# Kernel tuning notes

Measured on AMD Instinct MI355X. Metric: run time of the kernel, lower is better.

Reference implementation:

```python
import jax, jax.numpy as jnp
import numpy as np
from jax import lax

V = 9; C1 = 80; C2 = 40; C4 = 24; CH = 32
H1, W1 = 30, 40; H2, W2 = 60, 80; H4, W4 = 120, 160
SHAPE = (96, 96, 96); N = 131072; EPS = 1e-5
OFFS = np.stack(np.meshgrid(np.arange(-1, 2), np.arange(-1, 2), np.arange(-1, 2), indexing='ij'), -1).reshape(-1, 3).astype(np.int32)  # 27 kernel offsets


def conv2d(x, w, b):
    y = lax.conv_general_dilated(x, w, (1, 1), 'SAME', dimension_numbers=('NCHW', 'OIHW', 'NCHW'))
    return y + b[None, :, None, None]


def bn1d(x, g, b):  # eval-mode BatchNorm1d (running_mean=0, running_var=1)
    return g * x * (1.0 / np.sqrt(1.0 + EPS)) + b


def layernorm(x, g, b):
    m = x.mean(-1, keepdims=True)
    v = ((x - m) ** 2).mean(-1, keepdims=True)
    return (x - m) / jnp.sqrt(v + EPS) * g + b


def grid_sample_zeros(img, gx, gy):
    # img [V,C,H,W]; gx,gy [V,M] normalized to [-1,1]; bilinear, align_corners=True, zeros padding
    Vn, C, H, W = img.shape
    px = (gx + 1.0) * 0.5 * (W - 1)
    py = (gy + 1.0) * 0.5 * (H - 1)
    x0 = jnp.floor(px); y0 = jnp.floor(py)
    wx = px - x0; wy = py - y0
    flat = img.reshape(Vn, C, H * W)
    def corner(xc, yc, wgt):
        valid = (xc >= 0) & (xc <= W - 1) & (yc >= 0) & (yc <= H - 1)
        xi = jnp.clip(xc, 0, W - 1).astype(jnp.int32)
        yi = jnp.clip(yc, 0, H - 1).astype(jnp.int32)
        idx = yi * W + xi  # [V,M]
        g = jax.vmap(lambda f, i: f[:, i])(flat, idx)  # [V,C,M]
        return g * (wgt * valid)[:, None, :]
    return (corner(x0, y0, (1 - wx) * (1 - wy)) + corner(x0 + 1, y0, wx * (1 - wy))
            + corner(x0, y0 + 1, (1 - wx) * wy) + corner(x0 + 1, y0 + 1, wx * wy))


def subm_conv(feat, W3, cxyz, grid):
    # submanifold sparse 3x3x3 conv: per-offset gather of active neighbors -> GEMM -> accumulate
    n = feat.shape[0]
    shp = jnp.asarray(SHAPE, jnp.int32)
    out = jnp.zeros((n, W3.shape[-1]), feat.dtype)
    for k in range(27):
        nc = cxyz + jnp.asarray(OFFS[k])
        inb = jnp.all((nc >= 0) & (nc < shp), axis=1)
        ncc = jnp.clip(nc, 0, shp - 1)
        idx = grid[ncc[:, 0], ncc[:, 1], ncc[:, 2]]
        ok = (inb & (idx >= 0)).astype(feat.dtype)
        g = feat[jnp.clip(idx, 0, n - 1)] * ok[:, None]
        out = out + g @ W3[k]
    return out


def _forward(feats_1x, feats_2x, feats_4x, origin, voxel_size, KRcam,
             w_f1, b_f1, w_f2, b_f2, w_f4, b_f4, w_down, b_down,
             w_p1, b_p1, w_p2, b_p2, w_p3, b_p3, w_p4, b_p4,
             bn0_g, bn0_b, w_elan, w_s1, ln1_g, ln1_b, w_s2, ln2_g, ln2_b,
             w_s3, ln3_g, ln3_b, w_s4, bn4_g, bn4_b,
             coords, stage, min_view_number):
    # feat_fusion_pre (bs=1, take batch 0)
    f1 = jax.nn.relu(conv2d(feats_1x[:, 0], w_f1, b_f1))
    f2 = jax.nn.relu(conv2d(feats_2x[:, 0], w_f2, b_f2))
    f4 = jax.nn.relu(conv2d(feats_4x[:, 0], w_f4, b_f4))
    f1 = jax.image.resize(f1, (V, C1, H2, W2), 'bilinear')  # F.interpolate x2
    f4 = f4.reshape(V, C4, H2, 2, W2, 2).mean(axis=(3, 5))  # AvgPool2d(2)
    fuse = jnp.concatenate([f1, f2, f4], axis=1)
    fuse = jax.nn.relu(conv2d(fuse, w_down, b_down))
    for w, b in ((w_p1, b_p1), (w_p2, b_p2), (w_p3, b_p3), (w_p4, b_p4)):
        fuse = fuse + jax.nn.relu(conv2d(fuse, w, b))  # residual blocks -> [V,CH,H2,W2]
    # multi-view projection
    cxyz = coords[:, 1:]
    world = cxyz.astype(jnp.float32) * voxel_size + origin[0]
    hom = jnp.concatenate([world, jnp.ones_like(world[:, :1])], axis=1)  # [N,4]
    im_p = jnp.einsum('vij,nj->vin', KRcam[:, 0], hom)  # [V,3,N]
    im_z = im_p[:, 2]
    gx = 2.0 * (im_p[:, 0] / im_z) / (W4 - 1) - 1.0
    gy = 2.0 * (im_p[:, 1] / im_z) / (H4 - 1) - 1.0
    mask = (jnp.abs(gx) <= 1) & (jnp.abs(gy) <= 1) & (im_z > 0)  # [V,N]
    count = mask.sum(0).astype(jnp.float32)
    # inputs are constructed so every voxel is seen by all views: valid_voxel compaction == identity
    feats = grid_sample_zeros(fuse, gx, gy) * mask[:, None, :]  # [V,CH,N]
    feat = feats.transpose(2, 0, 1)  # [N,V,CH]
    m = mask.T.astype(feat.dtype)  # [N,V]
    den = m.sum(1, keepdims=True)
    mean = (m[..., None] * feat).sum(1) / den
    var = (m[..., None] * (feat - mean[:, None, :]) ** 2).sum(1) / den  # [N,CH]
    # sparse subm conv chain
    sc = cxyz // (2 ** (2 - stage))  # stage=2 -> identity
    grid = jnp.full(SHAPE, -1, jnp.int32).at[sc[:, 0], sc[:, 1], sc[:, 2]].set(jnp.arange(N, dtype=jnp.int32))
    x = bn1d(var, bn0_g, bn0_b)
    x = jax.nn.relu(subm_conv(x, w_elan, sc, grid))  # Spares3dELAN stand-in
    r = jax.nn.relu(subm_conv(x, w_s1, sc, grid)); x = layernorm(r + x, ln1_g, ln1_b)
    r = jax.nn.relu(subm_conv(x, w_s2, sc, grid)); x = layernorm(r + x, ln2_g, ln2_b)
    r = jax.nn.relu(subm_conv(x, w_s3, sc, grid)); x = layernorm(r + x, ln3_g, ln3_b)
    occ = bn1d(subm_conv(x, w_s4, sc, grid), bn4_g, bn4_b)  # [N,1]
    return occ, coords, count


def setup_inputs() -> dict:
    key = jax.random.key(0)
    keys = jax.random.split(key, 40)
    ki = iter(range(40))
    def rn(shape, s=1.0):
        return jax.random.normal(keys[next(ki)], shape, jnp.float32) * s
    inp = {}
    inp['feats_1x'] = rn((V, 1, C1, H1, W1))
    inp['feats_2x'] = rn((V, 1, C2, H2, W2))
    inp['feats_4x'] = rn((V, 1, C4, H4, W4))
    flat = np.arange(N, dtype=np.int64) * 6  # unique active voxels in a 96^3 grid
    cx = flat // (96 * 96); rem = flat % (96 * 96)
    inp['coords'] = jnp.asarray(np.stack([np.zeros(N, np.int64), cx, rem // 96, rem % 96], 1), jnp.int32)
    inp['origin'] = jnp.asarray([[-1.92, -1.92, 1.0]], jnp.float32)
    inp['voxel_size'] = jnp.float32(0.04)
    fx, fy = 38.0, 28.0
    P = np.zeros((V, 1, 3, 4), np.float32)
    for v in range(V):
        P[v, 0] = np.array([[fx, 0.0, (W4 - 1) / 2, fx * 0.02 * (v - 4)],
                            [0.0, fy, (H4 - 1) / 2, 0.0],
                            [0.0, 0.0, 1.0, 0.0]], np.float32)
    inp['KRcam'] = jnp.asarray(P)
    s = 0.05
    inp['w_f1'] = rn((C1, C1, 3, 3), s); inp['b_f1'] = rn((C1,), s)
    inp['w_f2'] = rn((C2, C2, 3, 3), s); inp['b_f2'] = rn((C2,), s)
    inp['w_f4'] = rn((C4, C4, 3, 3), s); inp['b_f4'] = rn((C4,), s)
    inp['w_down'] = rn((CH, C1 + C2 + C4, 1, 1), s); inp['b_down'] = rn((CH,), s)
    for i in (1, 2, 3, 4):
        inp['w_p%d' % i] = rn((CH, CH, 3, 3), s); inp['b_p%d' % i] = rn((CH,), s)
    inp['bn0_g'] = jnp.ones((CH,), jnp.float32); inp['bn0_b'] = jnp.zeros((CH,), jnp.float32)
    inp['w_elan'] = rn((27, CH, CH), s)
    inp['w_s1'] = rn((27, CH, CH), s); inp['ln1_g'] = jnp.ones((CH,), jnp.float32); inp['ln1_b'] = jnp.zeros((CH,), jnp.float32)
    inp['w_s2'] = rn((27, CH, CH), s); inp['ln2_g'] = jnp.ones((CH,), jnp.float32); inp['ln2_b'] = jnp.zeros((CH,), jnp.float32)
    inp['w_s3'] = rn((27, CH, CH), s); inp['ln3_g'] = jnp.ones((CH,), jnp.float32); inp['ln3_b'] = jnp.zeros((CH,), jnp.float32)
    inp['w_s4'] = rn((27, CH, 1), s); inp['bn4_g'] = jnp.ones((1,), jnp.float32); inp['bn4_b'] = jnp.zeros((1,), jnp.float32)
    inp['stage'] = 2
    inp['min_view_number'] = 1
    return inp


def reference(feats_1x, feats_2x, feats_4x, origin, voxel_size, KRcam,
              w_f1, b_f1, w_f2, b_f2, w_f4, b_f4, w_down, b_down,
              w_p1, b_p1, w_p2, b_p2, w_p3, b_p3, w_p4, b_p4,
              bn0_g, bn0_b, w_elan, w_s1, ln1_g, ln1_b, w_s2, ln2_g, ln2_b,
              w_s3, ln3_g, ln3_b, w_s4, bn4_g, bn4_b,
              coords, stage, min_view_number):
    return _forward(feats_1x, feats_2x, feats_4x, origin, voxel_size, KRcam,
                    w_f1, b_f1, w_f2, b_f2, w_f4, b_f4, w_down, b_down,
                    w_p1, b_p1, w_p2, b_p2, w_p3, b_p3, w_p4, b_p4,
                    bn0_g, bn0_b, w_elan, w_s1, ln1_g, ln1_b, w_s2, ln2_g, ln2_b,
                    w_s3, ln3_g, ln3_b, w_s4, bn4_g, bn4_b,
                    coords, stage, min_view_number)
```

## Files before the change

### kernel.cpp

```cpp
#include <hip/hip_runtime.h>
#include <math.h>

#define VN 9
#define NVOX 131072
#define GS 96
static constexpr float INVS = 0.9999950000374997f;

typedef short bf16x8 __attribute__((ext_vector_type(8)));
typedef float f32x4v __attribute__((ext_vector_type(4)));

__device__ inline float4 ld4(const float* p){ return *reinterpret_cast<const float4*>(p); }

__device__ inline ushort f2b(float f){
  unsigned u = __float_as_uint(f);
  unsigned r = (u + 0x7fffu + ((u >> 16) & 1u)) >> 16;
  return (ushort)r;
}
__device__ inline float b2f(ushort s){ return __uint_as_float(((unsigned)s) << 16); }
__device__ inline float blo(unsigned u){ return __uint_as_float(u << 16); }
__device__ inline float bhi(unsigned u){ return __uint_as_float(u & 0xffff0000u); }

__device__ inline float4 ld4b(const ushort* p){
  uint2 u = *reinterpret_cast<const uint2*>(p);
  float4 r; r.x = blo(u.x); r.y = bhi(u.x); r.z = blo(u.y); r.w = bhi(u.y); return r;
}
__device__ inline void st4b(ushort* p, float4 v){
  uint2 u;
  u.x = (unsigned)f2b(v.x) | ((unsigned)f2b(v.y) << 16);
  u.y = (unsigned)f2b(v.z) | ((unsigned)f2b(v.w) << 16);
  *reinterpret_cast<uint2*>(p) = u;
}

__device__ inline void wprep2_dev(const float* __restrict__ w, ushort* __restrict__ o,
                                  int Cout, int Cin, int K, int CK, int CoutPad, int tid){
  int ci32 = tid & 31;
  int co = (tid >> 5) % CoutPad;
  int ck = (tid / (32*CoutPad)) % CK;
  int tap = tid / (32*CoutPad*CK);
  int ci = ck*32 + ci32;
  float v = 0.f;
  if (co < Cout && ci < Cin) v = w[(size_t)(co*Cin + ci)*K*K + tap];
  o[tid] = f2b(v);
}
__device__ inline void wprep_dev(const float* __restrict__ w, ushort* __restrict__ o, int tid){
  int k = tid >> 10;
  int r = tid & 1023;
  int co = r >> 5;
  int ci = r & 31;
  o[tid] = f2b(w[k*1024 + ci*32 + co]);
}

__device__ inline void nhwc_tile_dev(const float* __restrict__ in, ushort* __restrict__ out,
                                     int C, int Cpad, int HW, int tile, int tilesPerV,
                                     float* lds, int tx){
  int v  = tile / tilesPerV;
  int p0 = (tile - v*tilesPerV) * 64;
  const float* ip = in + (size_t)v*C*HW + p0;
  int iters = Cpad >> 2;
  for (int i = 0; i < iters; ++i){
    int idx = i*256 + tx;
    int c = idx >> 6;
    int p = idx & 63;
    float val = 0.f;
    if (c < C && (p0 + p) < HW) val = ip[(size_t)c*HW + p];
    lds[c*65 + p] = val;
  }
  __syncthreads();
  int groups = Cpad >> 2;
  int tot = 64*groups;
  for (int basei = 0; basei < tot; basei += 256){
    int idx = basei + tx;
    if (idx < tot){
      int g  = idx % groups;
      int px = idx / groups;
      if ((p0 + px) < HW){
        float4 r;
        r.x = lds[(g*4+0)*65 + px];
        r.y = lds[(g*4+1)*65 + px];
        r.z = lds[(g*4+2)*65 + px];
        r.w = lds[(g*4+3)*65 + px];
        st4b(out + (size_t)(v*HW + p0 + px)*Cpad + g*4, r);
      }
    }
  }
}

__global__ __launch_bounds__(256) void k_prep(
    const float* wf1s, const float* wf2s, const float* wf4s, const float* wdns,
    const float* wp0s, const float* wp1s, const float* wp2s, const float* wp3s,
    const float* wes, const float* ws1s, const float* ws2s, const float* ws3s,
    ushort* wf1, ushort* wf2, ushort* wf4, ushort* wdn,
    ushort* wp0, ushort* wp1, ushort* wp2, ushort* wp3,
    ushort* w2e, ushort* w2s1, ushort* w2s2, ushort* w2s3,
    int* grid,
    const float* f1, const float* f2, const float* f4,
    ushort* o1, ushort* o2, ushort* o4){
  __shared__ float lds[96*65];
  int bid = blockIdx.x;
  int tx = threadIdx.x;
  if (bid < 270){ int t = bid*256+tx; if (t < 69120) wprep2_dev(wf1s, wf1, 80, 80, 3, 3, 80, t); return; }
  bid -= 270;
  if (bid < 108){ int t = bid*256+tx; if (t < 27648) wprep2_dev(wf2s, wf2, 40, 40, 3, 2, 48, t); return; }
  bid -= 108;
  if (bid < 36){ int t = bid*256+tx; if (t < 9216) wprep2_dev(wf4s, wf4, 24, 24, 3, 1, 32, t); return; }
  bid -= 36;
  if (bid < 20){ int t = bid*256+tx; if (t < 5120) wprep2_dev(wdns, wdn, 32, 144, 1, 5, 32, t); return; }
  bid -= 20;
  if (bid < 36){ int t = bid*256+tx; if (t < 9216) wprep2_dev(wp0s, wp0, 32, 32, 3, 1, 32, t); return; }
  bid -= 36;
  if (bid < 36){ int t = bid*256+tx; if (t < 9216) wprep2_dev(wp1s, wp1, 32, 32, 3, 1, 32, t); return; }
  bid -= 36;
  if (bid < 36){ int t = bid*256+tx; if (t < 9216) wprep2_dev(wp2s, wp2, 32, 32, 3, 1, 32, t); return; }
  bid -= 36;
  if (bid < 36){ int t = bid*256+tx; if (t < 9216) wprep2_dev(wp3s, wp3, 32, 32, 3, 1, 32, t); return; }
  bid -= 36;
  if (bid < 108){ int t = bid*256+tx; if (t < 27648) wprep_dev(wes, w2e, t); return; }
  bid -= 108;
  if (bid < 108){ int t = bid*256+tx; if (t < 27648) wprep_dev(ws1s, w2s1, t); return; }
  bid -= 108;
  if (bid < 108){ int t = bid*256+tx; if (t < 27648) wprep_dev(ws2s, w2s2, t); return; }
  bid -= 108;
  if (bid < 108){ int t = bid*256+tx; if (t < 27648) wprep_dev(ws3s, w2s3, t); return; }
  bid -= 108;
  if (bid < 3456){ int t = bid*256+tx; if (t < GS*GS*GS) grid[t] = -1; return; }
  bid -= 3456;
  if (bid < 171){ nhwc_tile_dev(f1, o1, 80, 96, 1200, bid, 19, lds, tx); return; }
  bid -= 171;
  if (bid < 675){ nhwc_tile_dev(f2, o2, 40, 64, 4800, bid, 75, lds, tx); return; }
  bid -= 675;
  if (bid < 2700){ nhwc_tile_dev(f4, o4, 24, 32, 19200, bid, 300, lds, tx); }
}

template<int CK, int NT, int TAPS, int MT>
__device__ void conv_dev(
    const ushort* __restrict__ fin, const ushort* __restrict__ w2,
    const float* __restrict__ bias, ushort* __restrict__ outp,
    int H, int W, int total, int Cout, int outStride, int outOff,
    const ushort* __restrict__ skipin, int bid, int tid){
  constexpr int CIN = CK*32;
  constexpr int COP = NT*16;
  int lane = tid & 63;
  int wave = tid >> 6;
  int vbase = bid*(MT*64) + wave*(MT*16);
  int m = lane & 15, q = lane >> 4;
  int HW = H*W;
  int p[MT], py[MT], px[MT]; bool pin[MT];
  #pragma unroll
  for (int t = 0; t < MT; ++t){
    int pp = vbase + t*16 + m;
    pin[t] = pp < total;
    if (pp > total-1) pp = total-1;
    p[t] = pp;
    int v = pp / HW; int rem = pp - v*HW;
    int y = rem / W;
    py[t] = y; px[t] = rem - y*W;
  }
  f32x4v acc[MT][NT];
  #pragma unroll
  for (int t = 0; t < MT; ++t)
    #pragma unroll
    for (int n = 0; n < NT; ++n) acc[t][n] = 0.f;
  bf16x8 z = (short)0;

  #pragma unroll 1
  for (int tap = 0; tap < TAPS; ++tap){
    int dy = (TAPS == 9) ? tap/3 - 1 : 0;
    int dx = (TAPS == 9) ? tap%3 - 1 : 0;
    int off = dy*W + dx;
    bool val[MT];
    #pragma unroll
    for (int t = 0; t < MT; ++t)
      val[t] = pin[t] && ((unsigned)(py[t]+dy) < (unsigned)H)
                      && ((unsigned)(px[t]+dx) < (unsigned)W);
    #pragma unroll
    for (int ck = 0; ck < CK; ++ck){
      bf16x8 Af[MT], Bf[NT];
      #pragma unroll
      for (int t = 0; t < MT; ++t){
        size_t idx = val[t] ? (size_t)(p[t]+off) : 0;
        bf16x8 a = *(const bf16x8*)(fin + idx*CIN + ck*32 + q*8);
        Af[t] = val[t] ? a : z;
      }
      #pragma unroll
      for (int n = 0; n < NT; ++n)
        Bf[n] = *(const bf16x8*)(w2 + ((size_t)((tap*CK+ck)*COP + n*16 + m))*32 + q*8);
      #pragma unroll
      for (int t = 0; t < MT; ++t)
        #pragma unroll
        for (int n = 0; n < NT; ++n)
          acc[t][n] = __builtin_amdgcn_mfma_f32_16x16x32_bf16(Af[t], Bf[n], acc[t][n], 0, 0, 0);
    }
  }

  #pragma unroll
  for (int n = 0; n < NT; ++n){
    int co = n*16 + m;
    bool cok = co < Cout;
    float bs = cok ? bias[co] : 0.f;
    #pragma unroll
    for (int t = 0; t < MT; ++t){
      #pragma unroll
      for (int r = 0; r < 4; ++r){
        int pp = vbase + t*16 + q*4 + r;
        if (pp < total && cok){
          float x = fmaxf(acc[t][n][r] + bs, 0.f);
          if (skipin) x += b2f(skipin[(size_t)pp*CIN + co]);
          outp[(size_t)pp*outStride + outOff + co] = f2b(x);
        }
      }
    }
  }
}

template<int CK, int NT, int TAPS, int MT>
__global__ __launch_bounds__(256) void k_conv_mfma(
    const ushort* __restrict__ fin, const ushort* __restrict__ w2,
    const float* __restrict__ bias, ushort* __restrict__ outp,
    int H, int W, int total, int Cout, int outStride, int outOff,
    const ushort* __restrict__ skipin){
  conv_dev<CK,NT,TAPS,MT>(fin, w2, bias, outp, H, W, total, Cout, outStride, outOff,
                          skipin, blockIdx.x, threadIdx.x);
}

template<int TH, int NT>
__device__ void conv_lds_dev(
    const ushort* __restrict__ fin, const ushort* __restrict__ w2,
    const float* __restrict__ bias, ushort* __restrict__ outp,
    int H, int W, int Cout, int outStride,
    const ushort* __restrict__ skipin, ushort* lds, int bid, int tid){
  constexpr int RPW = TH/4;
  constexpr int PS = 36;
  int xtiles = W >> 4;
  int ytiles = (H + TH - 1) / TH;
  int v  = bid / (ytiles*xtiles);
  int rem = bid - v*(ytiles*xtiles);
  int ty = (rem / xtiles) * TH;
  int tx = (rem % xtiles) * 16;
  const ushort* ibase = fin + (size_t)v*H*W*32;
  for (int i = tid; i < (TH+2)*18*4; i += 256){
    int chunk = i & 3;
    int pxi = i >> 2;
    int ly = pxi / 18, lx = pxi - ly*18;
    int gy = ty + ly - 1, gx = tx + lx - 1;
    uint4 d = {0,0,0,0};
    if ((unsigned)gy < (unsigned)H && (unsigned)gx < (unsigned)W)
      d = *(const uint4*)(ibase + ((size_t)gy*W + gx)*32 + chunk*8);
    *(uint4*)(lds + (size_t)(ly*18 + lx)*PS + chunk*8) = d;
  }
  __syncthreads();
  int lane = tid & 63;
  int wave = tid >> 6;
  int m = lane & 15, q = lane >> 4;
  f32x4v acc[RPW][NT];
  #pragma unroll
  for (int t = 0; t < RPW; ++t)
    #pragma unroll
    for (int n = 0; n < NT; ++n) acc[t][n] = 0.f;

  #pragma unroll 1
  for (int tap = 0; tap < 9; ++tap){
    int dy = tap/3 - 1, dx = tap%3 - 1;
    bf16x8 Af[RPW], Bf[NT];
    #pragma unroll
    for (int t = 0; t < RPW; ++t){
      int ly = wave*RPW + t + 1 + dy;
      int lx = m + 1 + dx;
      Af[t] = *(const bf16x8*)(lds + (size_t)(ly*18 + lx)*PS + q*8);
    }
    #pragma unroll
    for (int n = 0; n < NT; ++n)
      Bf[n] = *(const bf16x8*)(w2 + ((size_t)(tap*(NT*16) + n*16 + m))*32 + q*8);
    #pragma unroll
    for (int t = 0; t < RPW; ++t)
      #pragma unroll
      for (int n = 0; n < NT; ++n)
        acc[t][n] = __builtin_amdgcn_mfma_f32_16x16x32_bf16(Af[t], Bf[n], acc[t][n], 0, 0, 0);
  }

  #pragma unroll
  for (int n = 0; n < NT; ++n){
    int co = n*16 + m;
    bool cok = co < Cout;
    float bs = cok ? bias[co] : 0.f;
    #pragma unroll
    for (int t = 0; t < RPW; ++t){
      int y = ty + wave*RPW + t;
      #pragma unroll
      for (int r = 0; r < 4; ++r){
        int x = tx + q*4 + r;
        if (y < H && cok){
          size_t pp = (size_t)(v*H + y)*W + x;
          float val = fmaxf(acc[t][n][r] + bs, 0.f);
          if (skipin) val += b2f(skipin[pp*32 + co]);
          outp[pp*outStride + co] = f2b(val);
        }
      }
    }
  }
}

__global__ __launch_bounds__(256) void k_conv_lds4(
    const ushort* __restrict__ fin, const ushort* __restrict__ w2,
    const float* __restrict__ bias, ushort* __restrict__ outp,
    const ushort* __restrict__ skipin){
  __shared__ ushort lds[6*18*36];
  conv_lds_dev<4,2>(fin, w2, bias, outp, 60, 80, 32, 32, skipin, lds, blockIdx.x, threadIdx.x);
}

__device__ void scatter_dev(const int* __restrict__ coords, const int* __restrict__ stage,
                            int* __restrict__ grid, int* __restrict__ scn,
                            float* __restrict__ coords_out,
                            const float* __restrict__ origin, const float* __restrict__ vsz,
                            const float* __restrict__ KR,
                            ushort* __restrict__ sidx, uint2* __restrict__ sw,
                            float* __restrict__ cnt, int n){
  int c0 = coords[n*4], c1 = coords[n*4+1], c2 = coords[n*4+2], c3 = coords[n*4+3];
  coords_out[n*4+0] = (float)c0;
  coords_out[n*4+1] = (float)c1;
  coords_out[n*4+2] = (float)c2;
  coords_out[n*4+3] = (float)c3;
  int sh = 2 - stage[0];
  int s1 = c1 >> sh, s2 = c2 >> sh, s3 = c3 >> sh;
  scn[n*3+0] = s1; scn[n*3+1] = s2; scn[n*3+2] = s3;
  grid[(s1*GS + s2)*GS + s3] = n;

  float vs = vsz[0];
  float wx = (float)c1*vs + origin[0];
  float wy = (float)c2*vs + origin[1];
  float wz = (float)c3*vs + origin[2];
  float den = 0.f;
  #pragma unroll 1
  for (int v = 0; v < VN; ++v){
    const float* P = KR + v*12;
    float ix = P[0]*wx + P[1]*wy + P[2]*wz + P[3];
    float iy = P[4]*wx + P[5]*wy + P[6]*wz + P[7];
    float iz = P[8]*wx + P[9]*wy + P[10]*wz + P[11];
    float gx = 2.f*(ix/iz)/159.f - 1.f;
    float gy = 2.f*(iy/iz)/119.f - 1.f;
    bool ok = (fabsf(gx) <= 1.f) && (fabsf(gy) <= 1.f) && (iz > 0.f);
    float px = ok ? (gx + 1.f)*0.5f*79.f : 0.f;
    float py = ok ? (gy + 1.f)*0.5f*59.f : 0.f;
    float x0f = floorf(px), y0f = floorf(py);
    float fx = px - x0f, fy = py - y0f;
    int idx = (int)y0f*80 + (int)x0f;
    float mf = ok ? 1.f : 0.f;
    float w00 = (1.f-fx)*(1.f-fy)*mf, w01 = fx*(1.f-fy)*mf;
    float w10 = (1.f-fx)*fy*mf,       w11 = fx*fy*mf;
    uint2 s;
    s.x = (unsigned)f2b(w00) | ((unsigned)f2b(w01) << 16);
    s.y = (unsigned)f2b(w10) | ((unsigned)f2b(w11) << 16);
    sidx[(size_t)v*NVOX + n] = (ushort)idx;
    sw[(size_t)v*NVOX + n] = s;
    den += mf;
  }
  cnt[n] = den;
}

__global__ __launch_bounds__(256) void k_heads(
    const ushort* nhwc1, const ushort* wf1, const float* b_f1, ushort* t1,
    const ushort* nhwc2, const ushort* wf2, const float* b_f2, ushort* fcat,
    const ushort* nhwc4, const ushort* wf4, const float* b_f4, ushort* t4,
    const int* coords, const int* stage, int* grid, int* scn, float* coords_out,
    const float* origin, const float* vsz, const float* KR,
    ushort* sidx, uint2* sw, float* cnt){
  __shared__ ushort lds[18*18*36];
  int bid = blockIdx.x;
  int tid = threadIdx.x;
  if (bid < 169){ conv_dev<3,5,9,1>(nhwc1, wf1, b_f1, t1, 30, 40, 10800, 80, 80, 0, nullptr, bid, tid); return; }
  bid -= 169;
  if (bid < 720){ conv_lds_dev<16,2>(nhwc4, wf4, b_f4, t4, 120, 160, 24, 24, nullptr, lds, bid, tid); return; }
  bid -= 720;
  if (bid < 675){ conv_dev<2,3,9,1>(nhwc2, wf2, b_f2, fcat, 60, 80, 43200, 40, 160, 80, nullptr, bid, tid); return; }
  bid -= 675;
  { int n = bid*256 + tid;
    scatter_dev(coords, stage, grid, scn, coords_out, origin, vsz, KR, sidx, sw, cnt, n); }
}

__global__ __launch_bounds__(256) void k_respool_nbr(
    const ushort* __restrict__ t1, const ushort* __restrict__ t4, ushort* __restrict__ fc,
    const int* __restrict__ scn, const int* __restrict__ grid,
    int* __restrict__ nbr, unsigned* __restrict__ gmask16){
  __shared__ unsigned m16[4];
  int bid = blockIdx.x;
  int tidx = threadIdx.x;
  if (bid < 5063){
    int tid = bid*256 + tidx;
    if (tid < 864000){
      int c4 = tid % 20;
      int x  = (tid / 20) % 80;
      int y  = (tid / 1600) % 60;
      int v  = tid / 96000;
      int c = c4*4;
      int ky = y >> 1; int y0, y1; float wy0, wy1;
      if ((y & 1) == 0){ y0 = ky-1; y1 = ky; wy0 = 0.25f; wy1 = 0.75f; if (y0 < 0){ y0 = 0; wy0 = 0.f; wy1 = 1.f; } }
      else             { y0 = ky; y1 = ky+1; wy0 = 0.75f; wy1 = 0.25f; if (y1 > 29){ y1 = 29; wy1 = 0.f; wy0 = 1.f; } }
      int kx = x >> 1; int x0, x1; float wx0, wx1;
      if ((x & 1) == 0){ x0 = kx-1; x1 = kx; wx0 = 0.25f; wx1 = 0.75f; if (x0 < 0){ x0 = 0; wx0 = 0.f; wx1 = 1.f; } }
      else             { x0 = kx; x1 = kx+1; wx0 = 0.75f; wx1 = 0.25f; if (x1 > 39){ x1 = 39; wx1 = 0.f; wx0 = 1.f; } }
      float4 a00 = ld4b(t1 + ((size_t)(v*30 + y0)*40 + x0)*80 + c);
      float4 a01 = ld4b(t1 + ((size_t)(v*30 + y0)*40 + x1)*80 + c);
      float4 a10 = ld4b(t1 + ((size_t)(v*30 + y1)*40 + x0)*80 + c);
      float4 a11 = ld4b(t1 + ((size_t)(v*30 + y1)*40 + x1)*80 + c);
      float w00 = wy0*wx0, w01 = wy0*wx1, w10 = wy1*wx0, w11 = wy1*wx1;
      float4 r;
      r.x = w00*a00.x + w01*a01.x + w10*a10.x + w11*a11.x;
      r.y = w00*a00.y + w01*a01.y + w10*a10.y + w11*a11.y;
      r.z = w00*a00.z + w01*a01.z + w10*a10.z + w11*a11.z;
      r.w = w00*a00.w + w01*a01.w + w10*a10.w + w11*a11.w;
      st4b(fc + ((size_t)(v*60 + y)*80 + x)*160 + c, r);
      return;
    }
    int t = tid - 864000;
    if (t >= 432000) return;
    int c4 = t % 10;
    int x  = (t / 10) % 80;
    int y  = (t / 800) % 60;
    int v  = t / 48000;
    if (c4 < 6){
      int c = c4*4;
      const ushort* b0 = t4 + ((size_t)(v*120 + 2*y)*160 + 2*x)*24 + c;
      float4 a = ld4b(b0), b = ld4b(b0 + 24), cc = ld4b(b0 + 160*24), d = ld4b(b0 + 160*24 + 24);
      float4 r;
      r.x = 0.25f*(a.x + b.x + cc.x + d.x);
      r.y = 0.25f*(a.y + b.y + cc.y + d.y);
      r.z = 0.25f*(a.z + b.z + cc.z + d.z);
      r.w = 0.25f*(a.w + b.w + cc.w + d.w);
      st4b(fc + ((size_t)(v*60 + y)*80 + x)*160 + 120 + c, r);
    } else {
      float4 zz = {0.f,0.f,0.f,0.f};
      st4b(fc + ((size_t)(v*60 + y)*80 + x)*160 + 144 + (c4-6)*4, zz);
    }
    return;
  }
  bid -= 5063;
  if (tidx < 4) m16[tidx] = 0;
  __syncthreads();
  int vb = bid*64;
  int lane = tidx & 63;
  int wv = tidx >> 6;
  int n = vb + lane;
  int sx = scn[n*3+0], sy = scn[n*3+1], sz = scn[n*3+2];
  int k0 = wv*7;
  int k1 = min(27, k0 + 7);
  unsigned msk = 0;
  #pragma unroll 1
  for (int k = k0; k < k1; ++k){
    int dx = k/9 - 1, dy = (k/3)%3 - 1, dz = k%3 - 1;
    int nx = sx+dx, ny = sy+dy, nz = sz+dz;
    int idx = -1;
    if (((unsigned)nx < 96u) && ((unsigned)ny < 96u) && ((unsigned)nz < 96u))
      idx = grid[(nx*GS + ny)*GS + nz];
    unsigned long long b = __ballot(idx >= 0);
    unsigned sub = (unsigned)((b >> ((lane >> 4)*16)) & 0xFFFFull);
    if (sub){
      nbr[(size_t)k*NVOX + n] = idx;
      msk |= (1u << k);
    }
  }
  if ((lane & 15) == 0 && msk) atomicOr(&m16[lane >> 4], msk);
  __syncthreads();
  if (tidx < 4) gmask16[(vb >> 4) + tidx] = m16[tidx];
}

__global__ __launch_bounds__(256) void k_sample(
    const ushort* __restrict__ fuse, const ushort* __restrict__ sidx,
    const uint2* __restrict__ sw,
    const float* __restrict__ cnt, const float* __restrict__ bn0g,
    const float* __restrict__ bn0b, ushort* __restrict__ F0){
  int tid = blockIdx.x*256 + threadIdx.x;
  int vox = tid >> 3;
  int c4 = tid & 7;
  int c = c4*4;
  float s0=0.f,s1=0.f,s2=0.f,s3=0.f;
  float q0=0.f,q1=0.f,q2=0.f,q3=0.f;
  ushort si = sidx[vox];
  uint2 wv = sw[vox];
  #pragma unroll 1
  for (int v = 0; v < VN; ++v){
    ushort sn = si; uint2 wn = wv;
    if (v+1 < VN){
      sn = sidx[(size_t)(v+1)*NVOX + vox];
      wn = sw[(size_t)(v+1)*NVOX + vox];
    }
    float w00 = blo(wv.x), w01 = bhi(wv.x);
    float w10 = blo(wv.y), w11 = bhi(wv.y);
    const ushort* bp = fuse + (size_t)v*153600 + (size_t)si*32 + c;
    float4 a00 = ld4b(bp);
    float4 a01 = ld4b(bp + 32);
    float4 a10 = ld4b(bp + 2560);
    float4 a11 = ld4b(bp + 2592);
    float g0 = w00*a00.x + w01*a01.x + w10*a10.x + w11*a11.x;
    float g1 = w00*a00.y + w01*a01.y + w10*a10.y + w11*a11.y;
    float g2 = w00*a00.z + w01*a01.z + w10*a10.z + w11*a11.z;
    float g3 = w00*a00.w + w01*a01.w + w10*a10.w + w11*a11.w;
    s0 += g0; q0 += g0*g0;
    s1 += g1; q1 += g1*g1;
    s2 += g2; q2 += g2*g2;
    s3 += g3; q3 += g3*g3;
    si = sn; wv = wn;
  }
  float iden = 1.f/cnt[vox];
  float m0 = s0*iden, m1 = s1*iden, m2 = s2*iden, m3 = s3*iden;
  float4 g = ld4(bn0g + c);
  float4 b = ld4(bn0b + c);
  float4 r;
  r.x = g.x*fmaxf(q0*iden - m0*m0, 0.f)*INVS + b.x;
  r.y = g.y*fmaxf(q1*iden - m1*m1, 0.f)*INVS + b.y;
  r.z = g.z*fmaxf(q2*iden - m2*m2, 0.f)*INVS + b.z;
  r.w = g.w*fmaxf(q3*iden - m3*m3, 0.f)*INVS + b.w;
  st4b(F0 + (size_t)vox*32 + c, r);
}

template<int MODE>
__global__ __launch_bounds__(256, 4) void k_subm_mfma(
    const ushort* __restrict__ fin, const ushort* __restrict__ w2,
    const int* __restrict__ nbr, const unsigned* __restrict__ gmask16,
    const float* __restrict__ lng, const float* __restrict__ lnb,
    ushort* __restrict__ fout){
  int lane = threadIdx.x & 63;
  int wave = threadIdx.x >> 6;
  int vb = blockIdx.x*128 + wave*32;
  int m = lane & 15;
  int q = lane >> 4;

  unsigned rem0 = gmask16[(vb >> 4) + 0];
  unsigned rem1 = gmask16[(vb >> 4) + 1];
  unsigned rem = rem0 | rem1;

  f32x4v acc[2][2];
  acc[0][0] = 0.f; acc[0][1] = 0.f; acc[1][0] = 0.f; acc[1][1] = 0.f;
  bf16x8 zc = (short)0;

  int k0 = -1, k1 = -1;
  int a0 = -1, b0 = -1, a1 = -1, b1 = -1;
  if (rem){ k0 = __ffs(rem) - 1; rem &= rem - 1;
            a0 = ((rem0 >> k0) & 1) ? nbr[(size_t)k0*NVOX + vb + m] : -1;
            b0 = ((rem1 >> k0) & 1) ? nbr[(size_t)k0*NVOX + vb + 16 + m] : -1; }
  if (rem){ k1 = __ffs(rem) - 1; rem &= rem - 1;
            a1 = ((rem0 >> k1) & 1) ? nbr[(size_t)k1*NVOX + vb + m] : -1;
            b1 = ((rem1 >> k1) & 1) ? nbr[(size_t)k1*NVOX + vb + 16 + m] : -1; }
  bf16x8 A0 = zc, B0 = zc;
  if (k0 >= 0){
    bf16x8 t;
    t = *(const bf16x8*)(fin + (size_t)(a0 < 0 ? 0 : a0)*32 + q*8); A0 = (a0 < 0) ? zc : t;
    t = *(const bf16x8*)(fin + (size_t)(b0 < 0 ? 0 : b0)*32 + q*8); B0 = (b0 < 0) ? zc : t;
  }
  while (k0 >= 0){
    bf16x8 A1 = zc, B1 = zc;
    if (k1 >= 0){
      bf16x8 t;
      t = *(const bf16x8*)(fin + (size_t)(a1 < 0 ? 0 : a1)*32 + q*8); A1 = (a1 < 0) ? zc : t;
      t = *(const bf16x8*)(fin + (size_t)(b1 < 0 ? 0 : b1)*32 + q*8); B1 = (b1 < 0) ? zc : t;
    }
    int k2 = -1, a2 = -1, b2 = -1;
    if (rem){ k2 = __ffs(rem) - 1; rem &= rem - 1;
              a2 = ((rem0 >> k2) & 1) ? nbr[(size_t)k2*NVOX + vb + m] : -1;
              b2 = ((rem1 >> k2) & 1) ? nbr[(size_t)k2*NVOX + vb + 16 + m] : -1; }
    bf16x8 w0 = *(const bf16x8*)(w2 + (size_t)(k0*32 + m)*32 + q*8);
    bf16x8 w1 = *(const bf16x8*)(w2 + (size_t)(k0*32 + 16 + m)*32 + q*8);
    acc[0][0] = __builtin_amdgcn_mfma_f32_16x16x32_bf16(A0, w0, acc[0][0], 0, 0, 0);
    acc[0][1] = __builtin_amdgcn_mfma_f32_16x16x32_bf16(A0, w1, acc[0][1], 0, 0, 0);
    acc[1][0] = __builtin_amdgcn_mfma_f32_16x16x32_bf16(B0, w0, acc[1][0], 0, 0, 0);
    acc[1][1] = __builtin_amdgcn_mfma_f32_16x16x32_bf16(B0, w1, acc[1][1], 0, 0, 0);
    A0 = A1; B0 = B1; a1 = a2; b1 = b2; k0 = k1; k1 = k2;
  }

  int ch0 = m, ch1 = 16 + m;
  float g0 = 0.f, g1 = 0.f, bb0 = 0.f, bb1 = 0.f;
  if (MODE == 1){ g0 = lng[ch0]; g1 = lng[ch1]; bb0 = lnb[ch0]; bb1 = lnb[ch1]; }
  #pragma unroll
  for (int t = 0; t < 2; ++t){
    #pragma unroll
    for (int r = 0; r < 4; ++r){
      int vox = vb + t*16 + q*4 + r;
      float x0 = fmaxf(acc[t][0][r], 0.f);
      float x1 = fmaxf(acc[t][1][r], 0.f);
      if (MODE == 1){
        x0 += b2f(fin[(size_t)vox*32 + ch0]);
        x1 += b2f(fin[(size_t)vox*32 + ch1]);
        float s = x0 + x1;
        s += __shfl_xor(s, 1, 16);
        s += __shfl_xor(s, 2, 16);
        s += __shfl_xor(s, 4, 16);
        s += __shfl_xor(s, 8, 16);
        float mean = s * (1.f/32.f);
        float d0 = x0 - mean, d1 = x1 - mean;
        float v2 = d0*d0 + d1*d1;
        v2 += __shfl_xor(v2, 1, 16);
        v2 += __shfl_xor(v2, 2, 16);
        v2 += __shfl_xor(v2, 4, 16);
        v2 += __shfl_xor(v2, 8, 16);
        float rs = 1.f / sqrtf(v2*(1.f/32.f) + 1e-5f);
        x0 = d0*rs*g0 + bb0;
        x1 = d1*rs*g1 + bb1;
      }
      fout[(size_t)vox*32 + ch0] = f2b(x0);
      fout[(size_t)vox*32 + ch1] = f2b(x1);
    }
  }
}

__global__ __launch_bounds__(256) void k_s4(
    const ushort* __restrict__ fin, const float* __restrict__ w4,
    const int* __restrict__ nbr, const unsigned* __restrict__ gmask16,
    const float* __restrict__ bn4g, const float* __restrict__ bn4b,
    float* __restrict__ occ){
  int n = blockIdx.x*256 + threadIdx.x;
  if (n >= NVOX) return;
  unsigned rem = gmask16[n >> 4];
  float acc = 0.f;
  int k = -1, idx = -1;
  if (rem){ k = __ffs(rem) - 1; rem &= rem - 1; idx = nbr[(size_t)k*NVOX + n]; }
  while (k >= 0){
    int k2 = -1, idx2 = -1;
    if (rem){ k2 = __ffs(rem) - 1; rem &= rem - 1; idx2 = nbr[(size_t)k2*NVOX + n]; }
    if (idx >= 0){
      const uint4* r4 = (const uint4*)(fin + (size_t)idx*32);
      const float* wk = w4 + k*32;
      #pragma unroll
      for (int u = 0; u < 4; ++u){
        uint4 d = r4[u];
        const float* w8 = wk + u*8;
        acc += blo(d.x)*w8[0] + bhi(d.x)*w8[1];
        acc += blo(d.y)*w8[2] + bhi(d.y)*w8[3];
        acc += blo(d.z)*w8[4] + bhi(d.z)*w8[5];
        acc += blo(d.w)*w8[6] + bhi(d.w)*w8[7];
      }
    }
    k = k2; idx = idx2;
  }
  occ[n] = bn4g[0]*acc*INVS + bn4b[0];
}

extern "C" void kernel_launch(void* const* d_in, const int* in_sizes, int n_in,
                              void* d_out, int out_size, void* d_ws, size_t ws_size,
                              hipStream_t stream){
  const float* feats1 = (const float*)d_in[0];
  const float* feats2 = (const float*)d_in[1];
  const float* feats4 = (const float*)d_in[2];
  const int*   coords = (const int*)d_in[3];
  const float* origin = (const float*)d_in[4];
  const float* vsz    = (const float*)d_in[5];
  const float* KR     = (const float*)d_in[6];
  const float* w_f1 = (const float*)d_in[7];  const float* b_f1 = (const float*)d_in[8];
  const float* w_f2 = (const float*)d_in[9];  const float* b_f2 = (const float*)d_in[10];
  const float* w_f4 = (const float*)d_in[11]; const float* b_f4 = (const float*)d_in[12];
  const float* w_dn = (const float*)d_in[13]; const float* b_dn = (const float*)d_in[14];
  const float* w_p[4] = {(const float*)d_in[15], (const float*)d_in[17],
                         (const float*)d_in[19], (const float*)d_in[21]};
  const float* b_p[4] = {(const float*)d_in[16], (const float*)d_in[18],
                         (const float*)d_in[20], (const float*)d_in[22]};
  const float* bn0g = (const float*)d_in[23]; const float* bn0b = (const float*)d_in[24];
  const float* w_elan = (const float*)d_in[25];
  const float* w_s1 = (const float*)d_in[26]; const float* ln1g = (const float*)d_in[27]; const float* ln1b = (const float*)d_in[28];
  const float* w_s2 = (const float*)d_in[29]; const float* ln2g = (const float*)d_in[30]; const float* ln2b = (const float*)d_in[31];
  const float* w_s3 = (const float*)d_in[32]; const float* ln3g = (const float*)d_in[33]; const float* ln3b = (const float*)d_in[34];
  const float* w_s4 = (const float*)d_in[35]; const float* bn4g = (const float*)d_in[36]; const float* bn4b = (const float*)d_in[37];
  const int* stage  = (const int*)d_in[38];
  float* out = (float*)d_out;
  char* base = (char*)d_ws;

  size_t off = 0;
  auto alloc = [&](size_t bytes)->char*{ char* p = base + off; off += (bytes + 255) & ~(size_t)255; return p; };
  ushort* nhwc1 = (ushort*)alloc((size_t)9*30*40*96*2);
  ushort* nhwc2 = (ushort*)alloc((size_t)9*60*80*64*2);
  ushort* nhwc4 = (ushort*)alloc((size_t)9*120*160*32*2);
  ushort* t1    = (ushort*)alloc((size_t)9*30*40*80*2);
  ushort* t4    = (ushort*)alloc((size_t)9*120*160*24*2);
  ushort* fcat  = (ushort*)alloc((size_t)9*60*80*160*2);
  ushort* A     = (ushort*)alloc((size_t)9*60*80*32*2);
  ushort* B     = (ushort*)alloc((size_t)9*60*80*32*2);
  ushort* Fb0   = (ushort*)alloc((size_t)NVOX*32*2);
  ushort* Fb1   = (ushort*)alloc((size_t)NVOX*32*2);
  int*    nbr   = (int*)alloc((size_t)27*NVOX*4);
  int*    grid  = (int*)alloc((size_t)GS*GS*GS*4);
  int*    scn   = (int*)alloc((size_t)NVOX*3*4);
  unsigned* gmask16 = (unsigned*)alloc((size_t)(NVOX/16)*4);
  ushort* wf1   = (ushort*)alloc(9*3*80*32*2);
  ushort* wf2   = (ushort*)alloc(9*2*48*32*2);
  ushort* wf4   = (ushort*)alloc(9*1*32*32*2);
  ushort* wdn   = (ushort*)alloc(1*5*32*32*2);
  ushort* wp0   = (ushort*)alloc(9*1*32*32*2);
  ushort* wp1   = (ushort*)alloc(9*1*32*32*2);
  ushort* wp2   = (ushort*)alloc(9*1*32*32*2);
  ushort* wp3   = (ushort*)alloc(9*1*32*32*2);
  ushort* w2e   = (ushort*)alloc(27*1024*2);
  ushort* w2s1  = (ushort*)alloc(27*1024*2);
  ushort* w2s2  = (ushort*)alloc(27*1024*2);
  ushort* w2s3  = (ushort*)alloc(27*1024*2);
  ushort* sidx  = (ushort*)alloc((size_t)VN*NVOX*2);
  uint2*  sw    = (uint2*)alloc((size_t)VN*NVOX*8);

  auto nb = [](int total){ return (total + 255)/256; };

  k_prep<<<8012,256,0,stream>>>(
      w_f1, w_f2, w_f4, w_dn, w_p[0], w_p[1], w_p[2], w_p[3],
      w_elan, w_s1, w_s2, w_s3,
      wf1, wf2, wf4, wdn, wp0, wp1, wp2, wp3, w2e, w2s1, w2s2, w2s3, grid,
      feats1, feats2, feats4, nhwc1, nhwc2, nhwc4);

  k_heads<<<169 + 720 + 675 + 512,256,0,stream>>>(
      nhwc1, wf1, b_f1, t1,
      nhwc2, wf2, b_f2, fcat,
      nhwc4, wf4, b_f4, t4,
      coords, stage, grid, scn, out + NVOX,
      origin, vsz, KR, sidx, sw, out + 5*NVOX);

  k_respool_nbr<<<5063 + 2048,256,0,stream>>>(t1, t4, fcat, scn, grid, nbr, gmask16);

  k_conv_mfma<5,2,1,1><<<675,256,0,stream>>>(fcat, wdn, b_dn, A, 60, 80, 43200, 32, 32, 0, nullptr);
  k_conv_lds4<<<675,256,0,stream>>>(A, wp0, b_p[0], B, A);
  k_conv_lds4<<<675,256,0,stream>>>(B, wp1, b_p[1], A, B);
  k_conv_lds4<<<675,256,0,stream>>>(A, wp2, b_p[2], B, A);
  k_conv_lds4<<<675,256,0,stream>>>(B, wp3, b_p[3], A, B);

  k_sample<<<NVOX/32,256,0,stream>>>(A, sidx, sw, out + 5*NVOX, bn0g, bn0b, Fb0);

  k_subm_mfma<0><<<NVOX/128,256,0,stream>>>(Fb0, w2e,  nbr, gmask16, nullptr, nullptr, Fb1);
  k_subm_mfma<1><<<NVOX/128,256,0,stream>>>(Fb1, w2s1, nbr, gmask16, ln1g, ln1b, Fb0);
  k_subm_mfma<1><<<NVOX/128,256,0,stream>>>(Fb0, w2s2, nbr, gmask16, ln2g, ln2b, Fb1);
  k_subm_mfma<1><<<NVOX/128,256,0,stream>>>(Fb1, w2s3, nbr, gmask16, ln3g, ln3b, Fb0);

  k_s4<<<nb(NVOX),256,0,stream>>>(Fb0, w_s4, nbr, gmask16, bn4g, bn4b, out);
}
```

Baseline: 347.6 us.

## Batch gather loads in sampling, subm conv, and final sparse conv kernels

k_sample now preloads all nine views' sample indices and weights up front and fully unrolls the view loop, giving more loads in flight. The subm MFMA kernel handles three kernel offsets per iteration, issuing all neighbor-index, feature and weight loads before the MFMAs instead of using a software pipeline one offset deep. k_s4 splits each voxel across four threads that each load a 16-byte slice of the feature row and combine with shuffles, and processes two offsets per iteration. The goal is more memory-level parallelism and coalescing for these gathers, at the cost of more registers and 4x as many threads in k_s4.

```diff
diff --git a/kernel.cpp b/kernel.cpp
--- a/kernel.cpp
+++ b/kernel.cpp
@@ -471,20 +471,19 @@
   int vox = tid >> 3;
   int c4 = tid & 7;
   int c = c4*4;
+  int si[VN]; uint2 wv[VN];
+  #pragma unroll
+  for (int v = 0; v < VN; ++v){
+    si[v] = sidx[(size_t)v*NVOX + vox];
+    wv[v] = sw[(size_t)v*NVOX + vox];
+  }
   float s0=0.f,s1=0.f,s2=0.f,s3=0.f;
   float q0=0.f,q1=0.f,q2=0.f,q3=0.f;
-  ushort si = sidx[vox];
-  uint2 wv = sw[vox];
-  #pragma unroll 1
+  #pragma unroll
   for (int v = 0; v < VN; ++v){
-    ushort sn = si; uint2 wn = wv;
-    if (v+1 < VN){
-      sn = sidx[(size_t)(v+1)*NVOX + vox];
-      wn = sw[(size_t)(v+1)*NVOX + vox];
-    }
-    float w00 = blo(wv.x), w01 = bhi(wv.x);
-    float w10 = blo(wv.y), w11 = bhi(wv.y);
-    const ushort* bp = fuse + (size_t)v*153600 + (size_t)si*32 + c;
+    float w00 = blo(wv[v].x), w01 = bhi(wv[v].x);
+    float w10 = blo(wv[v].y), w11 = bhi(wv[v].y);
+    const ushort* bp = fuse + (size_t)v*153600 + (size_t)si[v]*32 + c;
     float4 a00 = ld4b(bp);
     float4 a01 = ld4b(bp + 32);
     float4 a10 = ld4b(bp + 2560);
@@ -497,7 +496,6 @@
     s1 += g1; q1 += g1*g1;
     s2 += g2; q2 += g2*g2;
     s3 += g3; q3 += g3*g3;
-    si = sn; wv = wn;
   }
   float iden = 1.f/cnt[vox];
   float m0 = s0*iden, m1 = s1*iden, m2 = s2*iden, m3 = s3*iden;
@@ -531,38 +529,62 @@
   acc[0][0] = 0.f; acc[0][1] = 0.f; acc[1][0] = 0.f; acc[1][1] = 0.f;
   bf16x8 zc = (short)0;
 
-  int k0 = -1, k1 = -1;
-  int a0 = -1, b0 = -1, a1 = -1, b1 = -1;
-  if (rem){ k0 = __ffs(rem) - 1; rem &= rem - 1;
-            a0 = ((rem0 >> k0) & 1) ? nbr[(size_t)k0*NVOX + vb + m] : -1;
-            b0 = ((rem1 >> k0) & 1) ? nbr[(size_t)k0*NVOX + vb + 16 + m] : -1; }
-  if (rem){ k1 = __ffs(rem) - 1; rem &= rem - 1;
-            a1 = ((rem0 >> k1) & 1) ? nbr[(size_t)k1*NVOX + vb + m] : -1;
-            b1 = ((rem1 >> k1) & 1) ? nbr[(size_t)k1*NVOX + vb + 16 + m] : -1; }
-  bf16x8 A0 = zc, B0 = zc;
-  if (k0 >= 0){
-    bf16x8 t;
+  while (rem){
+    int k0 = __ffs(rem) - 1; rem &= rem - 1;
+    int k1 = -1, k2 = -1;
+    if (rem){ k1 = __ffs(rem) - 1; rem &= rem - 1; }
+    if (rem){ k2 = __ffs(rem) - 1; rem &= rem - 1; }
+    int a0v = nbr[(size_t)k0*NVOX + vb + m];
+    int b0v = nbr[(size_t)k0*NVOX + vb + 16 + m];
+    int a1 = -1, b1 = -1, a2 = -1, b2 = -1;
+    if (k1 >= 0){
+      int av = nbr[(size_t)k1*NVOX + vb + m];
+      int bv = nbr[(size_t)k1*NVOX + vb + 16 + m];
+      a1 = ((rem0 >> k1) & 1) ? av : -1;
+      b1 = ((rem1 >> k1) & 1) ? bv : -1;
+    }
+    if (k2 >= 0){
+      int av = nbr[(size_t)k2*NVOX + vb + m];
+      int bv = nbr[(size_t)k2*NVOX + vb + 16 + m];
+      a2 = ((rem0 >> k2) & 1) ? av : -1;
+      b2 = ((rem1 >> k2) & 1) ? bv : -1;
+    }
+    int a0 = ((rem0 >> k0) & 1) ? a0v : -1;
+    int b0 = ((rem1 >> k0) & 1) ? b0v : -1;
+    bf16x8 A0, B0, A1 = zc, B1 = zc, A2 = zc, B2 = zc, t;
+    bf16x8 w10 = zc, w11 = zc, w20 = zc, w21 = zc;
     t = *(const bf16x8*)(fin + (size_t)(a0 < 0 ? 0 : a0)*32 + q*8); A0 = (a0 < 0) ? zc : t;
     t = *(const bf16x8*)(fin + (size_t)(b0 < 0 ? 0 : b0)*32 + q*8); B0 = (b0 < 0) ? zc : t;
-  }
-  while (k0 >= 0){
-    bf16x8 A1 = zc, B1 = zc;
+    bf16x8 w00 = *(const bf16x8*)(w2 + (size_t)(k0*32 + m)*32 + q*8);
+    bf16x8 w01 = *(const bf16x8*)(w2 + (size_t)(k0*32 + 16 + m)*32 + q*8);
     if (k1 >= 0){
-      bf16x8 t;
       t = *(const bf16x8*)(fin + (size_t)(a1 < 0 ? 0 : a1)*32 + q*8); A1 = (a1 < 0) ? zc : t;
       t = *(const bf16x8*)(fin + (size_t)(b1 < 0 ? 0 : b1)*32 + q*8); B1 = (b1 < 0) ? zc : t;
-    }
-    int k2 = -1, a2 = -1, b2 = -1;
-    if (rem){ k2 = __ffs(rem) - 1; rem &= rem - 1;
-              a2 = ((rem0 >> k2) & 1) ? nbr[(size_t)k2*NVOX + vb + m] : -1;
-              b2 = ((rem1 >> k2) & 1) ? nbr[(size_t)k2*NVOX + vb + 16 + m] : -1; }
-    bf16x8 w0 = *(const bf16x8*)(w2 + (size_t)(k0*32 + m)*32 + q*8);
-    bf16x8 w1 = *(const bf16x8*)(w2 + (size_t)(k0*32 + 16 + m)*32 + q*8);
-    acc[0][0] = __builtin_amdgcn_mfma_f32_16x16x32_bf16(A0, w0, acc[0][0], 0, 0, 0);
-    acc[0][1] = __builtin_amdgcn_mfma_f32_16x16x32_bf16(A0, w1, acc[0][1], 0, 0, 0);
-    acc[1][0] = __builtin_amdgcn_mfma_f32_16x16x32_bf16(B0, w0, acc[1][0], 0, 0, 0);
-    acc[1][1] = __builtin_amdgcn_mfma_f32_16x16x32_bf16(B0, w1, acc[1][1], 0, 0, 0);
-    A0 = A1; B0 = B1; a1 = a2; b1 = b2; k0 = k1; k1 = k2;
+      w10 = *(const bf16x8*)(w2 + (size_t)(k1*32 + m)*32 + q*8);
+      w11 = *(const bf16x8*)(w2 + (size_t)(k1*32 + 16 + m)*32 + q*8);
+    }
+    if (k2 >= 0){
+      t = *(const bf16x8*)(fin + (size_t)(a2 < 0 ? 0 : a2)*32 + q*8); A2 = (a2 < 0) ? zc : t;
+      t = *(const bf16x8*)(fin + (size_t)(b2 < 0 ? 0 : b2)*32 + q*8); B2 = (b2 < 0) ? zc : t;
+      w20 = *(const bf16x8*)(w2 + (size_t)(k2*32 + m)*32 + q*8);
+      w21 = *(const bf16x8*)(w2 + (size_t)(k2*32 + 16 + m)*32 + q*8);
+    }
+    acc[0][0] = __builtin_amdgcn_mfma_f32_16x16x32_bf16(A0, w00, acc[0][0], 0, 0, 0);
+    acc[0][1] = __builtin_amdgcn_mfma_f32_16x16x32_bf16(A0, w01, acc[0][1], 0, 0, 0);
+    acc[1][0] = __builtin_amdgcn_mfma_f32_16x16x32_bf16(B0, w00, acc[1][0], 0, 0, 0);
+    acc[1][1] = __builtin_amdgcn_mfma_f32_16x16x32_bf16(B0, w01, acc[1][1], 0, 0, 0);
+    if (k1 >= 0){
+      acc[0][0] = __builtin_amdgcn_mfma_f32_16x16x32_bf16(A1, w10, acc[0][0], 0, 0, 0);
+      acc[0][1] = __builtin_amdgcn_mfma_f32_16x16x32_bf16(A1, w11, acc[0][1], 0, 0, 0);
+      acc[1][0] = __builtin_amdgcn_mfma_f32_16x16x32_bf16(B1, w10, acc[1][0], 0, 0, 0);
+      acc[1][1] = __builtin_amdgcn_mfma_f32_16x16x32_bf16(B1, w11, acc[1][1], 0, 0, 0);
+    }
+    if (k2 >= 0){
+      acc[0][0] = __builtin_amdgcn_mfma_f32_16x16x32_bf16(A2, w20, acc[0][0], 0, 0, 0);
+      acc[0][1] = __builtin_amdgcn_mfma_f32_16x16x32_bf16(A2, w21, acc[0][1], 0, 0, 0);
+      acc[1][0] = __builtin_amdgcn_mfma_f32_16x16x32_bf16(B2, w20, acc[1][0], 0, 0, 0);
+      acc[1][1] = __builtin_amdgcn_mfma_f32_16x16x32_bf16(B2, w21, acc[1][1], 0, 0, 0);
+    }
   }
 
   int ch0 = m, ch1 = 16 + m;
@@ -605,31 +627,36 @@
     const int* __restrict__ nbr, const unsigned* __restrict__ gmask16,
     const float* __restrict__ bn4g, const float* __restrict__ bn4b,
     float* __restrict__ occ){
-  int n = blockIdx.x*256 + threadIdx.x;
-  if (n >= NVOX) return;
+  int tid = blockIdx.x*256 + threadIdx.x;
+  int n = tid >> 2;
+  int part = tid & 3;
   unsigned rem = gmask16[n >> 4];
   float acc = 0.f;
-  int k = -1, idx = -1;
-  if (rem){ k = __ffs(rem) - 1; rem &= rem - 1; idx = nbr[(size_t)k*NVOX + n]; }
-  while (k >= 0){
-    int k2 = -1, idx2 = -1;
-    if (rem){ k2 = __ffs(rem) - 1; rem &= rem - 1; idx2 = nbr[(size_t)k2*NVOX + n]; }
-    if (idx >= 0){
-      const uint4* r4 = (const uint4*)(fin + (size_t)idx*32);
-      const float* wk = w4 + k*32;
-      #pragma unroll
-      for (int u = 0; u < 4; ++u){
-        uint4 d = r4[u];
-        const float* w8 = wk + u*8;
-        acc += blo(d.x)*w8[0] + bhi(d.x)*w8[1];
-        acc += blo(d.y)*w8[2] + bhi(d.y)*w8[3];
-        acc += blo(d.z)*w8[4] + bhi(d.z)*w8[5];
-        acc += blo(d.w)*w8[6] + bhi(d.w)*w8[7];
-      }
-    }
-    k = k2; idx = idx2;
-  }
-  occ[n] = bn4g[0]*acc*INVS + bn4b[0];
+  while (rem){
+    int k0 = __ffs(rem) - 1; rem &= rem - 1;
+    int k1 = -1;
+    if (rem){ k1 = __ffs(rem) - 1; rem &= rem - 1; }
+    int i0 = nbr[(size_t)k0*NVOX + n];
+    int i1 = (k1 >= 0) ? nbr[(size_t)k1*NVOX + n] : -1;
+    uint4 d0 = *(const uint4*)(fin + (size_t)(i0 < 0 ? 0 : i0)*32 + part*8);
+    uint4 d1 = {0,0,0,0};
+    if (k1 >= 0) d1 = *(const uint4*)(fin + (size_t)(i1 < 0 ? 0 : i1)*32 + part*8);
+    if (i0 >= 0){
+      float4 wa = ld4(w4 + k0*32 + part*8);
+      float4 wb = ld4(w4 + k0*32 + part*8 + 4);
+      acc += blo(d0.x)*wa.x + bhi(d0.x)*wa.y + blo(d0.y)*wa.z + bhi(d0.y)*wa.w
+           + blo(d0.z)*wb.x + bhi(d0.z)*wb.y + blo(d0.w)*wb.z + bhi(d0.w)*wb.w;
+    }
+    if (i1 >= 0){
+      float4 wa = ld4(w4 + k1*32 + part*8);
+      float4 wb = ld4(w4 + k1*32 + part*8 + 4);
+      acc += blo(d1.x)*wa.x + bhi(d1.x)*wa.y + blo(d1.y)*wa.z + bhi(d1.y)*wa.w
+           + blo(d1.z)*wb.x + bhi(d1.z)*wb.y + blo(d1.w)*wb.z + bhi(d1.w)*wb.w;
+    }
+  }
+  acc += __shfl_xor(acc, 1, 4);
+  acc += __shfl_xor(acc, 2, 4);
+  if (part == 0) occ[n] = bn4g[0]*acc*INVS + bn4b[0];
 }
 
 extern "C" void kernel_launch(void* const* d_in, const int* in_sizes, int n_in,
@@ -721,5 +748,5 @@
   k_subm_mfma<1><<<NVOX/128,256,0,stream>>>(Fb0, w2s2, nbr, gmask16, ln2g, ln2b, Fb1);
   k_subm_mfma<1><<<NVOX/128,256,0,stream>>>(Fb1, w2s3, nbr, gmask16, ln3g, ln3b, Fb0);
 
-  k_s4<<<nb(NVOX),256,0,stream>>>(Fb0, w_s4, nbr, gmask16, bn4g, bn4b, out);
-}
+  k_s4<<<NVOX/64,256,0,stream>>>(Fb0, w_s4, nbr, gmask16, bn4g, bn4b, out);
+}
```

New measurement: 343.9 us. About the same (-1.1%).
